# Kernel optimization log

Hardware: AMD Instinct MI355X
Metric: run time of the kernel (lower is better)

The kernel has to match this reference:

```python
import jax, jax.numpy as jnp
import numpy as np
import math

N_HEAD = 16  # from init_kwargs

def setup_inputs() -> dict:
    key = jax.random.key(0)
    ks = jax.random.split(key, 11)
    B, T, D = 2, 2048, 1024
    s = 0.02
    return {
        "q": jax.random.normal(ks[0], (B, T, D), jnp.float32),
        "k": jax.random.normal(ks[1], (B, T, D), jnp.float32),
        "v": jax.random.normal(ks[2], (B, T, D), jnp.float32),
        "Wq": jax.random.normal(ks[3], (D, D), jnp.float32) * s,
        "bq": jax.random.normal(ks[4], (D,), jnp.float32) * s,
        "Wk": jax.random.normal(ks[5], (D, D), jnp.float32) * s,
        "bk": jax.random.normal(ks[6], (D,), jnp.float32) * s,
        "Wv": jax.random.normal(ks[7], (D, D), jnp.float32) * s,
        "bv": jax.random.normal(ks[8], (D,), jnp.float32) * s,
        "Wc": jax.random.normal(ks[9], (D, D), jnp.float32) * s,
        "bc": jax.random.normal(ks[10], (D,), jnp.float32) * s,
    }

def reference(q, k, v, Wq, bq, Wk, bk, Wv, bv, Wc, bc):
    B, T, D = q.shape
    H = N_HEAD
    nd = D // H

    def proj(x, W, b):
        # torch Linear: x @ W.T + b; then split heads -> [b, h, t, nd]
        y = x @ W.T + b
        return y.reshape(B, T, H, nd).transpose(0, 2, 1, 3)

    qh = proj(q, Wq, bq)
    kh = proj(k, Wk, bk)
    vh = proj(v, Wv, bv)

    # scores: [b, h, t_q, t_k]
    z = jnp.einsum('bhqd,bhkd->bhqk', qh, kh) / math.sqrt(nd)
    mask = jnp.tril(jnp.ones((T, T), dtype=bool))  # causal
    z = jnp.where(mask, z, -jnp.inf)
    # NOTE: original uses nn.Softmax(dim=-2) -> softmax over the QUERY axis
    attn = jax.nn.softmax(z, axis=-2)
    out = jnp.einsum('bhqk,bhkd->bhqd', attn, vh)  # [b, h, t, nd]
    out = out.transpose(0, 2, 1, 3).reshape(B, T, D)
    return out @ Wc.T + bc
```

## Files before the change

### kernel.cpp

```cpp
#include <hip/hip_runtime.h>


#define Dd 1024
#define Tt 2048
#define Bb 2
#define Hh 16
#define NDh 64
#define Mm (Bb * Tt)

using u16 = unsigned short;
using u32 = unsigned int;
typedef __attribute__((ext_vector_type(8))) short bf16x8;
typedef __attribute__((ext_vector_type(4))) float f32x4;

__device__ __forceinline__ u16 f2bf(float f) {
  return (u16)((__float_as_uint(f) + 0x8000u) >> 16);
}
__device__ __forceinline__ void ldsdma16(const u16* g, u16* l) {
  __builtin_amdgcn_global_load_lds(
      (const __attribute__((address_space(1))) u32*)g,
      (__attribute__((address_space(3))) u32*)l, 16, 0, 0);
}
#define MFMA(a, b, c) __builtin_amdgcn_mfma_f32_16x16x32_bf16((a), (b), (c), 0, 0, 0)
__device__ __forceinline__ bf16x8 ldfrag(const u16* lds, int row, int kgrp) {
  return *(const bf16x8*)(lds + row * 64 + (((kgrp) ^ (row & 7)) * 8));
}

__global__ __launch_bounds__(256) void cvt_all(
    const float* __restrict__ w0, const float* __restrict__ w1,
    const float* __restrict__ w2, const float* __restrict__ w3,
    const float* __restrict__ xq, const float* __restrict__ xk,
    const float* __restrict__ xv,
    u16* __restrict__ Wb, u16* __restrict__ Qb, u16* __restrict__ Kb,
    u16* __restrict__ Vb, float* __restrict__ outz, float* __restrict__ lsumz)
{
  const int vid = blockIdx.x * 256 + threadIdx.x;
  const int seg = vid >> 18;
  const size_t off = (size_t)(vid & 0x3FFFF) * 4;
  const float* s;
  u16* d;
  if (seg < 4) {
    s = seg == 0 ? w0 : seg == 1 ? w1 : seg == 2 ? w2 : w3;
    d = Wb + (size_t)seg * Dd * Dd;
  } else {
    const int xi = (seg - 4) >> 2;
    const size_t xo = (size_t)((seg - 4) & 3) << 20;
    s = (xi == 0 ? xq : xi == 1 ? xk : xv) + xo;
    d = (xi == 0 ? Qb : xi == 1 ? Kb : Vb) + xo;
  }
  float4 f = *(const float4*)(s + off);
  ushort4 o;
  o.x = f2bf(f.x); o.y = f2bf(f.y); o.z = f2bf(f.z); o.w = f2bf(f.w);
  *(ushort4*)(d + off) = o;
  if (vid < Mm * Dd / 4)
    *(float4*)(outz + (size_t)vid * 4) = make_float4(0.f, 0.f, 0.f, 0.f);
  if (vid < Bb * Hh * Tt / 4)
    *(float4*)(lsumz + (size_t)vid * 4) = make_float4(0.f, 0.f, 0.f, 0.f);
}

__device__ __forceinline__ void gemm_body(
    const u16* __restrict__ X, const u16* __restrict__ WB,
    const float* __restrict__ bias, void* Yv, float oscale, int omode,
    int kc, int knum, u16* As, u16* Bs)
{
  const int t = threadIdx.x, lane = t & 63, w = t >> 6;
  const int col = lane & 15, quad = lane >> 4;
  const int m0 = blockIdx.x * 64, n0 = blockIdx.y * 128;
  const int wm = (w >> 1) * 32, wn = (w & 1) * 64;
  const int drr = lane >> 3, dsw = ((lane & 7) ^ drr) * 8;
  const int kbeg = (Dd / knum) * kc, kend = kbeg + Dd / knum;

  f32x4 acc[2][4] = {};

  for (int k0 = kbeg; k0 < kend; k0 += 64) {
    __syncthreads();
#pragma unroll
    for (int i = 0; i < 2; i++) {
      const int rr = w * 16 + i * 8;
      ldsdma16(X + (size_t)(m0 + rr + drr) * Dd + k0 + dsw, As + rr * 64);
    }
#pragma unroll
    for (int i = 0; i < 4; i++) {
      const int rr = w * 32 + i * 8;
      ldsdma16(WB + (size_t)(n0 + rr + drr) * Dd + k0 + dsw, Bs + rr * 64);
    }
    __syncthreads();
#pragma unroll
    for (int s = 0; s < 2; s++) {
      bf16x8 a[2], b[4];
#pragma unroll
      for (int i = 0; i < 2; i++)
        a[i] = ldfrag(As, wm + i * 16 + col, s * 4 + quad);
#pragma unroll
      for (int j = 0; j < 4; j++)
        b[j] = ldfrag(Bs, wn + j * 16 + col, s * 4 + quad);
#pragma unroll
      for (int i = 0; i < 2; i++)
#pragma unroll
        for (int j = 0; j < 4; j++)
          acc[i][j] = MFMA(a[i], b[j], acc[i][j]);
    }
  }

#pragma unroll
  for (int jt = 0; jt < 4; jt++) {
    const int n = n0 + wn + jt * 16 + col;
    const float bn = (omode == 2 && kc != 0) ? 0.f : bias[n];
    if (omode == 1) {
#pragma unroll
      for (int i = 0; i < 2; i++) {
        const int mg = m0 + wm + i * 16 + quad * 4;
        const int bb = mg >> 11, tl = mg & 2047;
        ushort4 o;
        o.x = f2bf(acc[i][jt][0] + bn);
        o.y = f2bf(acc[i][jt][1] + bn);
        o.z = f2bf(acc[i][jt][2] + bn);
        o.w = f2bf(acc[i][jt][3] + bn);
        *(ushort4*)((u16*)Yv + (size_t)bb * Dd * Tt + (size_t)n * Tt + tl) = o;
      }
    } else if (omode == 0) {
      u16* Y = (u16*)Yv;
#pragma unroll
      for (int i = 0; i < 2; i++)
#pragma unroll
        for (int r = 0; r < 4; r++) {
          const int m = m0 + wm + i * 16 + quad * 4 + r;
          Y[(size_t)m * Dd + n] = f2bf((acc[i][jt][r] + bn) * oscale);
        }
    } else {
      float* Y = (float*)Yv;
#pragma unroll
      for (int i = 0; i < 2; i++)
#pragma unroll
        for (int r = 0; r < 4; r++) {
          const int m = m0 + wm + i * 16 + quad * 4 + r;
          atomicAdd(&Y[(size_t)m * Dd + n], acc[i][jt][r] + bn);
        }
    }
  }
}

__global__ __launch_bounds__(256) void proj_qkv(
    const u16* __restrict__ Qb, const u16* __restrict__ Kb,
    const u16* __restrict__ Vb, const u16* __restrict__ Wb,
    const float* __restrict__ bq, const float* __restrict__ bk,
    const float* __restrict__ bv,
    u16* __restrict__ Qp, u16* __restrict__ Kp, u16* __restrict__ VtG)
{
  __shared__ u16 As[64 * 64];
  __shared__ u16 Bs[128 * 64];
  const int z = blockIdx.z;
  const u16* X = z == 0 ? Qb : z == 1 ? Kb : Vb;
  const u16* W = Wb + (size_t)z * Dd * Dd;
  const float* bias = z == 0 ? bq : z == 1 ? bk : bv;
  void* Y = z == 0 ? (void*)Qp : z == 1 ? (void*)Kp : (void*)VtG;
  gemm_body(X, W, bias, Y, z == 0 ? 0.125f : 1.0f, z == 2 ? 1 : 0, 0, 1, As, Bs);
}

__global__ __launch_bounds__(256) void gemm_final(
    const u16* __restrict__ Ctx, const u16* __restrict__ Wcb,
    const float* __restrict__ bc, float* __restrict__ out)
{
  __shared__ u16 As[64 * 64];
  __shared__ u16 Bs[128 * 64];
  gemm_body(Ctx, Wcb, bc, out, 1.0f, 2, blockIdx.z, 2, As, Bs);
}

__global__ __launch_bounds__(256) void attn_stats(
    const u16* __restrict__ Qp, const u16* __restrict__ Kp,
    float* __restrict__ lsum)
{
  __shared__ u16 Ks[128 * 64];
  __shared__ u16 Qs[64 * 64];
  const int t = threadIdx.x, lane = t & 63, w = t >> 6;
  const int col = lane & 15, quad = lane >> 4;
  const int bh = blockIdx.x, b = bh >> 4, h = bh & 15;
  const int j = blockIdx.y, tk0 = j * 128, c = blockIdx.z;
  const u16* Kbase = Kp + (size_t)b * Tt * Dd + h * NDh;
  const u16* Qbase = Qp + (size_t)b * Tt * Dd + h * NDh;
  const int drr = lane >> 3, dsw = ((lane & 7) ^ drr) * 8;

#pragma unroll
  for (int i = 0; i < 4; i++) {
    const int rr = w * 32 + i * 8;
    ldsdma16(Kbase + (size_t)(tk0 + rr + drr) * Dd + dsw, Ks + rr * 64);
  }
  __syncthreads();
  bf16x8 ka[2][2];
#pragma unroll
  for (int s2 = 0; s2 < 2; s2++) {
    const int row = w * 32 + s2 * 16 + col;
    ka[s2][0] = ldfrag(Ks, row, quad);
    ka[s2][1] = ldfrag(Ks, row, 4 + quad);
  }

  float l[2][4] = {};

  for (int d = 2 * j + c, i0 = 0; d < Tt / 64; d += 4, i0++) {
    const bool masked = (c < 2) && (i0 == 0);
    const int tq0 = d * 64;
    __syncthreads();
#pragma unroll
    for (int i = 0; i < 2; i++) {
      const int rr = w * 16 + i * 8;
      ldsdma16(Qbase + (size_t)(tq0 + rr + drr) * Dd + dsw, Qs + rr * 64);
    }
    __syncthreads();
#pragma unroll
    for (int jt = 0; jt < 4; jt++) {
      bf16x8 qb0 = ldfrag(Qs, jt * 16 + col, quad);
      bf16x8 qb1 = ldfrag(Qs, jt * 16 + col, 4 + quad);
      const int tq = tq0 + jt * 16 + col;
#pragma unroll
      for (int s2 = 0; s2 < 2; s2++) {
        f32x4 z = {};
        z = MFMA(ka[s2][0], qb0, z);
        z = MFMA(ka[s2][1], qb1, z);
#pragma unroll
        for (int r = 0; r < 4; r++) {
          float e = __expf(z[r]);
          if (masked) {
            const int tk = tk0 + w * 32 + s2 * 16 + quad * 4 + r;
            e = (tq >= tk) ? e : 0.f;
          }
          l[s2][r] += e;
        }
      }
    }
  }

#pragma unroll
  for (int s2 = 0; s2 < 2; s2++)
#pragma unroll
    for (int r = 0; r < 4; r++) {
      float s = l[s2][r];
#pragma unroll
      for (int m = 1; m < 16; m <<= 1) s += __shfl_xor(s, m);
      if (col == 0)
        atomicAdd(&lsum[(size_t)bh * Tt + tk0 + w * 32 + s2 * 16 + quad * 4 + r], s);
    }
}

__global__ __launch_bounds__(256) void attn_out(
    const u16* __restrict__ Qp, const u16* __restrict__ Kp,
    const u16* __restrict__ VtG, const float* __restrict__ lsum,
    u16* __restrict__ Ctx)
{
  __shared__ u16 QPs[64 * 64];
  __shared__ u16 Ks[64 * 64];
  __shared__ u16 Vts[64 * 64];
  __shared__ float srl[64];
  const int t = threadIdx.x, lane = t & 63, w = t >> 6;
  const int col = lane & 15, quad = lane >> 4;
  const int bh = blockIdx.x, b = bh >> 4, h = bh & 15;
  const int tq0 = (gridDim.y - 1 - blockIdx.y) * 64;
  const u16* Qbase = Qp + (size_t)b * Tt * Dd + h * NDh;
  const u16* Kbase = Kp + (size_t)b * Tt * Dd + h * NDh;
  const u16* Vbase = VtG + (size_t)b * Dd * Tt + (size_t)h * NDh * Tt;
  const int drr = lane >> 3, dsw = ((lane & 7) ^ drr) * 8;

#pragma unroll
  for (int i = 0; i < 2; i++) {
    const int rr = w * 16 + i * 8;
    ldsdma16(Qbase + (size_t)(tq0 + rr + drr) * Dd + dsw, QPs + rr * 64);
  }
  __syncthreads();
  bf16x8 qa[2];
  qa[0] = ldfrag(QPs, w * 16 + col, quad);
  qa[1] = ldfrag(QPs, w * 16 + col, 4 + quad);

  f32x4 o[4] = {};

  for (int tk0 = 0; tk0 <= tq0; tk0 += 64) {
    const bool masked = (tk0 == tq0);
    __syncthreads();
#pragma unroll
    for (int i = 0; i < 2; i++) {
      const int rr = w * 16 + i * 8;
      ldsdma16(Kbase + (size_t)(tk0 + rr + drr) * Dd + dsw, Ks + rr * 64);
      ldsdma16(Vbase + (size_t)(rr + drr) * Tt + tk0 + dsw, Vts + rr * 64);
    }
    if (t < 64) srl[t] = 1.0f / lsum[(size_t)bh * Tt + tk0 + t];
    __syncthreads();
#pragma unroll
    for (int jt = 0; jt < 4; jt++) {
      bf16x8 kb0 = ldfrag(Ks, jt * 16 + col, quad);
      bf16x8 kb1 = ldfrag(Ks, jt * 16 + col, 4 + quad);
      const int tkl = jt * 16 + col;
      const float rl = srl[tkl];
      f32x4 z = {};
      z = MFMA(qa[0], kb0, z);
      z = MFMA(qa[1], kb1, z);
#pragma unroll
      for (int r = 0; r < 4; r++) {
        const int row = w * 16 + quad * 4 + r;
        float p = __expf(z[r]) * rl;
        if (masked) p = (tkl <= row) ? p : 0.f;
        QPs[row * 64 + (((tkl >> 3) ^ (row & 7)) * 8) + (tkl & 7)] = f2bf(p);
      }
    }
    bf16x8 pa0 = ldfrag(QPs, w * 16 + col, quad);
    bf16x8 pa1 = ldfrag(QPs, w * 16 + col, 4 + quad);
#pragma unroll
    for (int dn = 0; dn < 4; dn++) {
      bf16x8 vb0 = ldfrag(Vts, dn * 16 + col, quad);
      bf16x8 vb1 = ldfrag(Vts, dn * 16 + col, 4 + quad);
      o[dn] = MFMA(pa0, vb0, o[dn]);
      o[dn] = MFMA(pa1, vb1, o[dn]);
    }
  }

#pragma unroll
  for (int dn = 0; dn < 4; dn++)
#pragma unroll
    for (int r = 0; r < 4; r++) {
      const int tq = tq0 + w * 16 + quad * 4 + r;
      Ctx[(size_t)(b * Tt + tq) * Dd + h * NDh + dn * 16 + col] = f2bf(o[dn][r]);
    }
}

extern "C" void kernel_launch(void* const* d_in, const int* in_sizes, int n_in,
                              void* d_out, int out_size, void* d_ws, size_t ws_size,
                              hipStream_t stream)
{
  const float* q  = (const float*)d_in[0];
  const float* k  = (const float*)d_in[1];
  const float* v  = (const float*)d_in[2];
  const float* Wq = (const float*)d_in[3];
  const float* bq = (const float*)d_in[4];
  const float* Wk = (const float*)d_in[5];
  const float* bk = (const float*)d_in[6];
  const float* Wv = (const float*)d_in[7];
  const float* bv = (const float*)d_in[8];
  const float* Wc = (const float*)d_in[9];
  const float* bc = (const float*)d_in[10];

  u16* Wb   = (u16*)d_ws;
  u16* Qp   = Wb + (size_t)4 * Dd * Dd;
  u16* Kp   = Qp + (size_t)Mm * Dd;
  u16* VtG  = Kp + (size_t)Mm * Dd;
  u16* Ctx  = VtG + (size_t)Mm * Dd;
  float* lsum = (float*)(Ctx + (size_t)Mm * Dd);
  u16* Qb   = (u16*)(lsum + (size_t)Bb * Hh * Tt);
  u16* Kb   = Qb + (size_t)Mm * Dd;
  u16* Vb   = Ctx;

  cvt_all<<<16384, 256, 0, stream>>>(Wq, Wk, Wv, Wc, q, k, v,
                                     Wb, Qb, Kb, Vb, (float*)d_out, lsum);
  proj_qkv<<<dim3(Mm / 64, Dd / 128, 3), 256, 0, stream>>>(
      Qb, Kb, Vb, Wb, bq, bk, bv, Qp, Kp, VtG);
  attn_stats<<<dim3(Bb * Hh, Tt / 128, 4), 256, 0, stream>>>(Qp, Kp, lsum);
  attn_out<<<dim3(Bb * Hh, Tt / 64), 256, 0, stream>>>(Qp, Kp, VtG, lsum, Ctx);
  gemm_final<<<dim3(Mm / 64, Dd / 128, 2), 256, 0, stream>>>(
      Ctx, Wb + (size_t)3 * Dd * Dd, bc, (float*)d_out);
}
```

Baseline: 260.1 us.

## Pair short and long causal query tiles per block and use hardware exp2

Each attn_out block now handles two query tiles, one near the start and one near the end of the sequence. This balances causal work across blocks and lets one K/V tile load serve both tiles, halving the grid. The Q projection scale is pre-multiplied by log2(e) so both attention kernels can call the raw v_exp_f32 instruction instead of __expf. In exchange the kernel holds more registers and LDS for the doubled accumulators and Q tiles, and runs fewer blocks.

```diff
diff --git a/kernel.cpp b/kernel.cpp
--- a/kernel.cpp
+++ b/kernel.cpp
@@ -7,6 +7,7 @@
 #define Hh 16
 #define NDh 64
 #define Mm (Bb * Tt)
+#define LOG2E 1.44269504f
 
 using u16 = unsigned short;
 using u32 = unsigned int;
@@ -15,6 +16,9 @@
 
 __device__ __forceinline__ u16 f2bf(float f) {
   return (u16)((__float_as_uint(f) + 0x8000u) >> 16);
+}
+__device__ __forceinline__ float exp2_hw(float x) {
+  float r; asm("v_exp_f32 %0, %1" : "=v"(r) : "v"(x)); return r;
 }
 __device__ __forceinline__ void ldsdma16(const u16* g, u16* l) {
   __builtin_amdgcn_global_load_lds(
@@ -154,7 +158,8 @@
   const u16* W = Wb + (size_t)z * Dd * Dd;
   const float* bias = z == 0 ? bq : z == 1 ? bk : bv;
   void* Y = z == 0 ? (void*)Qp : z == 1 ? (void*)Kp : (void*)VtG;
-  gemm_body(X, W, bias, Y, z == 0 ? 0.125f : 1.0f, z == 2 ? 1 : 0, 0, 1, As, Bs);
+  gemm_body(X, W, bias, Y, z == 0 ? 0.125f * LOG2E : 1.0f, z == 2 ? 1 : 0,
+            0, 1, As, Bs);
 }
 
 __global__ __launch_bounds__(256) void gemm_final(
@@ -218,7 +223,7 @@
         z = MFMA(ka[s2][1], qb1, z);
 #pragma unroll
         for (int r = 0; r < 4; r++) {
-          float e = __expf(z[r]);
+          float e = exp2_hw(z[r]);
           if (masked) {
             const int tk = tk0 + w * 32 + s2 * 16 + quad * 4 + r;
             e = (tq >= tk) ? e : 0.f;
@@ -246,14 +251,15 @@
     const u16* __restrict__ VtG, const float* __restrict__ lsum,
     u16* __restrict__ Ctx)
 {
-  __shared__ u16 QPs[64 * 64];
+  __shared__ u16 QPs[128 * 64];
   __shared__ u16 Ks[64 * 64];
   __shared__ u16 Vts[64 * 64];
   __shared__ float srl[64];
   const int t = threadIdx.x, lane = t & 63, w = t >> 6;
   const int col = lane & 15, quad = lane >> 4;
   const int bh = blockIdx.x, b = bh >> 4, h = bh & 15;
-  const int tq0 = (gridDim.y - 1 - blockIdx.y) * 64;
+  const int p = blockIdx.y;
+  const int tqA = p * 64, tqB = (31 - p) * 64;
   const u16* Qbase = Qp + (size_t)b * Tt * Dd + h * NDh;
   const u16* Kbase = Kp + (size_t)b * Tt * Dd + h * NDh;
   const u16* Vbase = VtG + (size_t)b * Dd * Tt + (size_t)h * NDh * Tt;
@@ -262,17 +268,20 @@
 #pragma unroll
   for (int i = 0; i < 2; i++) {
     const int rr = w * 16 + i * 8;
-    ldsdma16(Qbase + (size_t)(tq0 + rr + drr) * Dd + dsw, QPs + rr * 64);
+    ldsdma16(Qbase + (size_t)(tqA + rr + drr) * Dd + dsw, QPs + rr * 64);
+    ldsdma16(Qbase + (size_t)(tqB + rr + drr) * Dd + dsw, QPs + (64 + rr) * 64);
   }
   __syncthreads();
-  bf16x8 qa[2];
-  qa[0] = ldfrag(QPs, w * 16 + col, quad);
-  qa[1] = ldfrag(QPs, w * 16 + col, 4 + quad);
-
-  f32x4 o[4] = {};
-
-  for (int tk0 = 0; tk0 <= tq0; tk0 += 64) {
-    const bool masked = (tk0 == tq0);
+  bf16x8 qaA0 = ldfrag(QPs, w * 16 + col, quad);
+  bf16x8 qaA1 = ldfrag(QPs, w * 16 + col, 4 + quad);
+  bf16x8 qaB0 = ldfrag(QPs, 64 + w * 16 + col, quad);
+  bf16x8 qaB1 = ldfrag(QPs, 64 + w * 16 + col, 4 + quad);
+
+  f32x4 oA[4] = {}, oB[4] = {};
+
+  for (int tk0 = 0; tk0 <= tqB; tk0 += 64) {
+    const bool actA = (tk0 <= tqA);
+    const bool mA = (tk0 == tqA), mB = (tk0 == tqB);
     __syncthreads();
 #pragma unroll
     for (int i = 0; i < 2; i++) {
@@ -288,25 +297,54 @@
       bf16x8 kb1 = ldfrag(Ks, jt * 16 + col, 4 + quad);
       const int tkl = jt * 16 + col;
       const float rl = srl[tkl];
-      f32x4 z = {};
-      z = MFMA(qa[0], kb0, z);
-      z = MFMA(qa[1], kb1, z);
-#pragma unroll
-      for (int r = 0; r < 4; r++) {
-        const int row = w * 16 + quad * 4 + r;
-        float p = __expf(z[r]) * rl;
-        if (masked) p = (tkl <= row) ? p : 0.f;
-        QPs[row * 64 + (((tkl >> 3) ^ (row & 7)) * 8) + (tkl & 7)] = f2bf(p);
-      }
-    }
-    bf16x8 pa0 = ldfrag(QPs, w * 16 + col, quad);
-    bf16x8 pa1 = ldfrag(QPs, w * 16 + col, 4 + quad);
-#pragma unroll
-    for (int dn = 0; dn < 4; dn++) {
-      bf16x8 vb0 = ldfrag(Vts, dn * 16 + col, quad);
-      bf16x8 vb1 = ldfrag(Vts, dn * 16 + col, 4 + quad);
-      o[dn] = MFMA(pa0, vb0, o[dn]);
-      o[dn] = MFMA(pa1, vb1, o[dn]);
+      {
+        f32x4 z = {};
+        z = MFMA(qaB0, kb0, z);
+        z = MFMA(qaB1, kb1, z);
+#pragma unroll
+        for (int r = 0; r < 4; r++) {
+          const int row = w * 16 + quad * 4 + r;
+          float pv = exp2_hw(z[r]) * rl;
+          if (mB) pv = (tkl <= row) ? pv : 0.f;
+          QPs[(64 + row) * 64 + (((tkl >> 3) ^ (row & 7)) * 8) + (tkl & 7)] =
+              f2bf(pv);
+        }
+      }
+      if (actA) {
+        f32x4 z = {};
+        z = MFMA(qaA0, kb0, z);
+        z = MFMA(qaA1, kb1, z);
+#pragma unroll
+        for (int r = 0; r < 4; r++) {
+          const int row = w * 16 + quad * 4 + r;
+          float pv = exp2_hw(z[r]) * rl;
+          if (mA) pv = (tkl <= row) ? pv : 0.f;
+          QPs[row * 64 + (((tkl >> 3) ^ (row & 7)) * 8) + (tkl & 7)] = f2bf(pv);
+        }
+      }
+    }
+    bf16x8 paB0 = ldfrag(QPs, 64 + w * 16 + col, quad);
+    bf16x8 paB1 = ldfrag(QPs, 64 + w * 16 + col, 4 + quad);
+    if (actA) {
+      bf16x8 paA0 = ldfrag(QPs, w * 16 + col, quad);
+      bf16x8 paA1 = ldfrag(QPs, w * 16 + col, 4 + quad);
+#pragma unroll
+      for (int dn = 0; dn < 4; dn++) {
+        bf16x8 vb0 = ldfrag(Vts, dn * 16 + col, quad);
+        bf16x8 vb1 = ldfrag(Vts, dn * 16 + col, 4 + quad);
+        oB[dn] = MFMA(paB0, vb0, oB[dn]);
+        oB[dn] = MFMA(paB1, vb1, oB[dn]);
+        oA[dn] = MFMA(paA0, vb0, oA[dn]);
+        oA[dn] = MFMA(paA1, vb1, oA[dn]);
+      }
+    } else {
+#pragma unroll
+      for (int dn = 0; dn < 4; dn++) {
+        bf16x8 vb0 = ldfrag(Vts, dn * 16 + col, quad);
+        bf16x8 vb1 = ldfrag(Vts, dn * 16 + col, 4 + quad);
+        oB[dn] = MFMA(paB0, vb0, oB[dn]);
+        oB[dn] = MFMA(paB1, vb1, oB[dn]);
+      }
     }
   }
 
@@ -314,8 +352,10 @@
   for (int dn = 0; dn < 4; dn++)
 #pragma unroll
     for (int r = 0; r < 4; r++) {
-      const int tq = tq0 + w * 16 + quad * 4 + r;
-      Ctx[(size_t)(b * Tt + tq) * Dd + h * NDh + dn * 16 + col] = f2bf(o[dn][r]);
+      const int lrow = w * 16 + quad * 4 + r;
+      const int nn = h * NDh + dn * 16 + col;
+      Ctx[(size_t)(b * Tt + tqA + lrow) * Dd + nn] = f2bf(oA[dn][r]);
+      Ctx[(size_t)(b * Tt + tqB + lrow) * Dd + nn] = f2bf(oB[dn][r]);
     }
 }
 
@@ -350,7 +390,7 @@
   proj_qkv<<<dim3(Mm / 64, Dd / 128, 3), 256, 0, stream>>>(
       Qb, Kb, Vb, Wb, bq, bk, bv, Qp, Kp, VtG);
   attn_stats<<<dim3(Bb * Hh, Tt / 128, 4), 256, 0, stream>>>(Qp, Kp, lsum);
-  attn_out<<<dim3(Bb * Hh, Tt / 64), 256, 0, stream>>>(Qp, Kp, VtG, lsum, Ctx);
+  attn_out<<<dim3(Bb * Hh, Tt / 128), 256, 0, stream>>>(Qp, Kp, VtG, lsum, Ctx);
   gemm_final<<<dim3(Mm / 64, Dd / 128, 2), 256, 0, stream>>>(
       Ctx, Wb + (size_t)3 * Dd * Dd, bc, (float*)d_out);
 }
```

Measured after the change: 261.0 us. No clear change (+0.4%).

## Keep attention probabilities in registers and fold log2e into Q scale

Applied to the files above, without the earlier changes.

The attention-output kernel now computes S transposed (K as the A operand), so each lane's score accumulator directly forms a bf16x4 B-operand for a 16x16x16 MFMA against V. This removes the LDS round-trip for the probability tile, along with its scattered 16-bit stores. The Q projection scale is premultiplied by log2(e) so the hardware v_exp_f32 (exp2) replaces __expf in both the stats and output kernels. Probabilities are packed with v_cvt_pk_bf16_f32 and the output is written as ushort4. The trade-off is twice as many smaller MFMAs for PV, plus inline asm that depends on the ISA.

```diff
diff --git a/kernel.cpp b/kernel.cpp
--- a/kernel.cpp
+++ b/kernel.cpp
@@ -7,14 +7,23 @@
 #define Hh 16
 #define NDh 64
 #define Mm (Bb * Tt)
+#define LOG2E 1.44269504f
 
 using u16 = unsigned short;
 using u32 = unsigned int;
 typedef __attribute__((ext_vector_type(8))) short bf16x8;
+typedef __attribute__((ext_vector_type(4))) short bf16x4;
 typedef __attribute__((ext_vector_type(4))) float f32x4;
 
 __device__ __forceinline__ u16 f2bf(float f) {
   return (u16)((__float_as_uint(f) + 0x8000u) >> 16);
+}
+__device__ __forceinline__ float exp2_hw(float x) {
+  float r; asm("v_exp_f32 %0, %1" : "=v"(r) : "v"(x)); return r;
+}
+__device__ __forceinline__ u32 cvtpk(float lo, float hi) {
+  u32 r; asm("v_cvt_pk_bf16_f32 %0, %1, %2" : "=v"(r) : "v"(lo), "v"(hi));
+  return r;
 }
 __device__ __forceinline__ void ldsdma16(const u16* g, u16* l) {
   __builtin_amdgcn_global_load_lds(
@@ -22,8 +31,21 @@
       (__attribute__((address_space(3))) u32*)l, 16, 0, 0);
 }
 #define MFMA(a, b, c) __builtin_amdgcn_mfma_f32_16x16x32_bf16((a), (b), (c), 0, 0, 0)
+__device__ __forceinline__ f32x4 mfma16(bf16x4 a, bf16x4 b, f32x4 c) {
+#if __has_builtin(__builtin_amdgcn_mfma_f32_16x16x16bf16_1k)
+  return __builtin_amdgcn_mfma_f32_16x16x16bf16_1k(a, b, c, 0, 0, 0);
+#else
+  f32x4 d;
+  asm("v_mfma_f32_16x16x16_bf16 %0, %1, %2, %3"
+      : "=v"(d) : "v"(a), "v"(b), "0"(c));
+  return d;
+#endif
+}
 __device__ __forceinline__ bf16x8 ldfrag(const u16* lds, int row, int kgrp) {
   return *(const bf16x8*)(lds + row * 64 + (((kgrp) ^ (row & 7)) * 8));
+}
+__device__ __forceinline__ bf16x4 ldv4(const u16* lds, int row, int e0) {
+  return *(const bf16x4*)(lds + row * 64 + (((e0 >> 3) ^ (row & 7)) * 8) + (e0 & 7));
 }
 
 __global__ __launch_bounds__(256) void cvt_all(
@@ -154,7 +176,8 @@
   const u16* W = Wb + (size_t)z * Dd * Dd;
   const float* bias = z == 0 ? bq : z == 1 ? bk : bv;
   void* Y = z == 0 ? (void*)Qp : z == 1 ? (void*)Kp : (void*)VtG;
-  gemm_body(X, W, bias, Y, z == 0 ? 0.125f : 1.0f, z == 2 ? 1 : 0, 0, 1, As, Bs);
+  gemm_body(X, W, bias, Y, z == 0 ? 0.125f * LOG2E : 1.0f, z == 2 ? 1 : 0,
+            0, 1, As, Bs);
 }
 
 __global__ __launch_bounds__(256) void gemm_final(
@@ -218,7 +241,7 @@
         z = MFMA(ka[s2][1], qb1, z);
 #pragma unroll
         for (int r = 0; r < 4; r++) {
-          float e = __expf(z[r]);
+          float e = exp2_hw(z[r]);
           if (masked) {
             const int tk = tk0 + w * 32 + s2 * 16 + quad * 4 + r;
             e = (tq >= tk) ? e : 0.f;
@@ -246,7 +269,7 @@
     const u16* __restrict__ VtG, const float* __restrict__ lsum,
     u16* __restrict__ Ctx)
 {
-  __shared__ u16 QPs[64 * 64];
+  __shared__ u16 Qs[64 * 64];
   __shared__ u16 Ks[64 * 64];
   __shared__ u16 Vts[64 * 64];
   __shared__ float srl[64];
@@ -262,12 +285,11 @@
 #pragma unroll
   for (int i = 0; i < 2; i++) {
     const int rr = w * 16 + i * 8;
-    ldsdma16(Qbase + (size_t)(tq0 + rr + drr) * Dd + dsw, QPs + rr * 64);
+    ldsdma16(Qbase + (size_t)(tq0 + rr + drr) * Dd + dsw, Qs + rr * 64);
   }
   __syncthreads();
-  bf16x8 qa[2];
-  qa[0] = ldfrag(QPs, w * 16 + col, quad);
-  qa[1] = ldfrag(QPs, w * 16 + col, 4 + quad);
+  bf16x8 qa0 = ldfrag(Qs, w * 16 + col, quad);
+  bf16x8 qa1 = ldfrag(Qs, w * 16 + col, 4 + quad);
 
   f32x4 o[4] = {};
 
@@ -286,37 +308,40 @@
     for (int jt = 0; jt < 4; jt++) {
       bf16x8 kb0 = ldfrag(Ks, jt * 16 + col, quad);
       bf16x8 kb1 = ldfrag(Ks, jt * 16 + col, 4 + quad);
-      const int tkl = jt * 16 + col;
-      const float rl = srl[tkl];
       f32x4 z = {};
-      z = MFMA(qa[0], kb0, z);
-      z = MFMA(qa[1], kb1, z);
-#pragma unroll
-      for (int r = 0; r < 4; r++) {
-        const int row = w * 16 + quad * 4 + r;
-        float p = __expf(z[r]) * rl;
-        if (masked) p = (tkl <= row) ? p : 0.f;
-        QPs[row * 64 + (((tkl >> 3) ^ (row & 7)) * 8) + (tkl & 7)] = f2bf(p);
+      z = MFMA(kb0, qa0, z);
+      z = MFMA(kb1, qa1, z);
+      const f32x4 rl = *(const f32x4*)(srl + jt * 16 + quad * 4);
+      float p0 = exp2_hw(z[0]) * rl[0];
+      float p1 = exp2_hw(z[1]) * rl[1];
+      float p2 = exp2_hw(z[2]) * rl[2];
+      float p3 = exp2_hw(z[3]) * rl[3];
+      if (masked) {
+        const int tkb = jt * 16 + quad * 4, tq = w * 16 + col;
+        p0 = (tkb + 0 <= tq) ? p0 : 0.f;
+        p1 = (tkb + 1 <= tq) ? p1 : 0.f;
+        p2 = (tkb + 2 <= tq) ? p2 : 0.f;
+        p3 = (tkb + 3 <= tq) ? p3 : 0.f;
       }
-    }
-    bf16x8 pa0 = ldfrag(QPs, w * 16 + col, quad);
-    bf16x8 pa1 = ldfrag(QPs, w * 16 + col, 4 + quad);
-#pragma unroll
-    for (int dn = 0; dn < 4; dn++) {
-      bf16x8 vb0 = ldfrag(Vts, dn * 16 + col, quad);
-      bf16x8 vb1 = ldfrag(Vts, dn * 16 + col, 4 + quad);
-      o[dn] = MFMA(pa0, vb0, o[dn]);
-      o[dn] = MFMA(pa1, vb1, o[dn]);
-    }
-  }
-
-#pragma unroll
-  for (int dn = 0; dn < 4; dn++)
-#pragma unroll
-    for (int r = 0; r < 4; r++) {
-      const int tq = tq0 + w * 16 + quad * 4 + r;
-      Ctx[(size_t)(b * Tt + tq) * Dd + h * NDh + dn * 16 + col] = f2bf(o[dn][r]);
-    }
+      u32 pk01 = cvtpk(p0, p1), pk23 = cvtpk(p2, p3);
+      u32 pkv[2] = {pk01, pk23};
+      const bf16x4 pb = *(const bf16x4*)pkv;
+#pragma unroll
+      for (int dn = 0; dn < 4; dn++) {
+        const bf16x4 va = ldv4(Vts, dn * 16 + col, jt * 16 + quad * 4);
+        o[dn] = mfma16(va, pb, o[dn]);
+      }
+    }
+  }
+
+#pragma unroll
+  for (int dn = 0; dn < 4; dn++) {
+    ushort4 ov;
+    ov.x = f2bf(o[dn][0]); ov.y = f2bf(o[dn][1]);
+    ov.z = f2bf(o[dn][2]); ov.w = f2bf(o[dn][3]);
+    *(ushort4*)(Ctx + (size_t)(b * Tt + tq0 + w * 16 + col) * Dd +
+                h * NDh + dn * 16 + quad * 4) = ov;
+  }
 }
 
 extern "C" void kernel_launch(void* const* d_in, const int* in_sizes, int n_in,
```

Result: no change. 263.1 us (+1.2%).
